# Kernel optimization log

Hardware: AMD Instinct MI355X
Metric: run time of the kernel (lower is better)

## Reference

```python
import jax, jax.numpy as jnp
import numpy as np

N = 100000      # total nodes across the batch of graphs
E = 1600000     # total edges (avg degree 16)
D = 128         # dim_drug (== num_feature here)
L = 3           # layer_drug
G = 2048        # number of graphs in the batch
BN_EPS = 1e-5


def setup_inputs() -> dict:
    key = jax.random.key(0)
    ks = jax.random.split(key, 10)
    x = jax.random.normal(ks[0], (N, D), dtype=jnp.float32)
    edge_index = jax.random.randint(ks[1], (2, E), 0, N, dtype=jnp.int64)
    batch = jnp.sort(jax.random.randint(ks[2], (N,), 0, G, dtype=jnp.int64))
    s = 0.05
    W1 = jax.random.normal(ks[3], (L, D, D), dtype=jnp.float32) * s
    b1 = jax.random.normal(ks[4], (L, D), dtype=jnp.float32) * s
    W2 = jax.random.normal(ks[5], (L, D, D), dtype=jnp.float32) * s
    b2 = jax.random.normal(ks[6], (L, D), dtype=jnp.float32) * s
    gamma = jnp.ones((L, D), dtype=jnp.float32)
    beta = jnp.zeros((L, D), dtype=jnp.float32)
    return {"x": x, "edge_index": edge_index, "batch": batch,
            "W1": W1, "b1": b1, "W2": W2, "b2": b2,
            "gamma": gamma, "beta": beta}


def reference(x, edge_index, batch, W1, b1, W2, b2, gamma, beta):
    src, dst = edge_index[0], edge_index[1]
    h = x
    layer_outs = []
    for i in range(L):
        # GINConv, eps=0: MLP( (1+eps)*h + sum_{j->i} h_j )
        agg = jax.ops.segment_sum(h[src], dst, num_segments=N)  # [N, D]
        m = agg + h
        m = jax.nn.relu(m @ W1[i] + b1[i]) @ W2[i] + b2[i]       # 2-layer MLP
        m = jax.nn.relu(m)                                        # F.relu after conv
        # BatchNorm1d (training mode: batch stats over node dim, biased var)
        mean = jnp.mean(m, axis=0)
        var = jnp.mean((m - mean) ** 2, axis=0)
        h = gamma[i] * (m - mean) * jax.lax.rsqrt(var + BN_EPS) + beta[i]
        layer_outs.append(h)
    node_rep = jnp.concatenate(layer_outs, axis=1)  # JK 'cat' -> [N, L*D]
    return jax.ops.segment_max(node_rep, batch, num_segments=G)  # [G, L*D]
```

## Files before the change

kernel.cpp:

```cpp
#include <hip/hip_runtime.h>
#include <stdint.h>

#define NN 100000
#define NE 1600000
#define DD 128
#define NL 3
#define NG 2048
#define BN_EPS 1e-5f
#define CAP 56
#define GSH 9
#define GSZ 512
#define NGRP 196
#define GBINCAP 9216

typedef short s16x8 __attribute__((ext_vector_type(8)));
typedef float f32x4 __attribute__((ext_vector_type(4)));

__device__ __forceinline__ unsigned short f2bfu(float f) {
    union { float f; unsigned int i; } x; x.f = f;
    unsigned int r = x.i + 0x7fffu + ((x.i >> 16) & 1u);
    return (unsigned short)(r >> 16);
}
__device__ __forceinline__ float bfu2f(unsigned short u) {
    union { unsigned int i; float f; } x; x.i = ((unsigned int)u) << 16; return x.f;
}
__device__ __forceinline__ float uplo(unsigned int u) {
    union { unsigned int i; float f; } x; x.i = u << 16; return x.f;
}
__device__ __forceinline__ float uphi(unsigned int u) {
    union { unsigned int i; float f; } x; x.i = u & 0xffff0000u; return x.f;
}
__device__ __forceinline__ void add8(float* a, uint4 v) {
    a[0] += uplo(v.x); a[1] += uphi(v.x);
    a[2] += uplo(v.y); a[3] += uphi(v.y);
    a[4] += uplo(v.z); a[5] += uphi(v.z);
    a[6] += uplo(v.w); a[7] += uphi(v.w);
}
__device__ __forceinline__ unsigned int pack2(float a, float b) {
    return (unsigned int)f2bfu(a) | ((unsigned int)f2bfu(b) << 16);
}

__global__ __launch_bounds__(256) void k_cvt(
    const float* __restrict__ x, unsigned short* __restrict__ hb)
{
    int i = (blockIdx.x * 256 + threadIdx.x) * 4;
    if (i >= NN * DD) return;
    float4 v = *(const float4*)(x + i);
    ushort4 o;
    o.x = f2bfu(v.x); o.y = f2bfu(v.y); o.z = f2bfu(v.z); o.w = f2bfu(v.w);
    *(ushort4*)(hb + i) = o;
}

__global__ __launch_bounds__(256) void k_wtrans(
    const float* __restrict__ W1, const float* __restrict__ W2,
    unsigned short* __restrict__ Wt)
{
    int idx = blockIdx.x * 256 + threadIdx.x;
    if (idx >= 6 * DD * DD) return;
    int mat = idx >> 14;
    int r = idx & 16383;
    int n = r >> 7, k = r & 127;
    const float* src = (mat < 3) ? (W1 + mat * DD * DD) : (W2 + (mat - 3) * DD * DD);
    Wt[idx] = f2bfu(src[k * DD + n]);
}

__global__ __launch_bounds__(256) void k_bounds(
    const int* __restrict__ batch, int* __restrict__ start)
{
    int n = blockIdx.x * 256 + threadIdx.x;
    if (n >= NN) return;
    int bn = batch[n];
    bn = bn < 0 ? 0 : (bn > NG - 1 ? NG - 1 : bn);
    int bp;
    if (n == 0) bp = -1;
    else {
        bp = batch[n - 1];
        bp = bp < 0 ? 0 : (bp > NG - 1 ? NG - 1 : bp);
    }
    for (int g = bp + 1; g <= bn; ++g) start[g] = n;
    if (n == NN - 1) {
        for (int g = bn + 1; g <= NG; ++g) start[g] = NN;
    }
}

__global__ __launch_bounds__(256) void k_grp(
    const int* __restrict__ ei, int* __restrict__ gcnt,
    unsigned int* __restrict__ bins)
{
    __shared__ int hist[256];
    __shared__ int scn[256];
    __shared__ int exs[256];
    __shared__ int lofs[256];
    __shared__ int gbase[256];
    __shared__ unsigned int stage[4096];
    const int tid = threadIdx.x;
    hist[tid] = 0;
    __syncthreads();

    unsigned int pk[16];
    int gg[16];
    unsigned int vmask = 0;
    #pragma unroll
    for (int q = 0; q < 4; ++q) {
        long long e0 = (long long)blockIdx.x * 4096 + q * 1024 + tid * 4;
        if (e0 < NE) {
            const int* dp = ei + NE + e0;
            const int* sp = ei + e0;
            int dd_[4], ss_[4];
            dd_[0] = __builtin_nontemporal_load(dp + 0);
            dd_[1] = __builtin_nontemporal_load(dp + 1);
            dd_[2] = __builtin_nontemporal_load(dp + 2);
            dd_[3] = __builtin_nontemporal_load(dp + 3);
            ss_[0] = __builtin_nontemporal_load(sp + 0);
            ss_[1] = __builtin_nontemporal_load(sp + 1);
            ss_[2] = __builtin_nontemporal_load(sp + 2);
            ss_[3] = __builtin_nontemporal_load(sp + 3);
            #pragma unroll
            for (int i = 0; i < 4; ++i) {
                int dst = dd_[i], src = ss_[i];
                if ((unsigned)dst < NN && (unsigned)src < NN) {
                    int g = dst >> GSH;
                    int j = q * 4 + i;
                    pk[j] = ((unsigned)(dst & (GSZ - 1)) << 17) | (unsigned)src;
                    gg[j] = g;
                    atomicAdd(&hist[g], 1);
                    vmask |= 1u << j;
                }
            }
        }
    }
    __syncthreads();

    int v = hist[tid];
    scn[tid] = v;
    __syncthreads();
    #pragma unroll
    for (int off = 1; off < 256; off <<= 1) {
        int t = (tid >= off) ? scn[tid - off] : 0;
        __syncthreads();
        scn[tid] += t;
        __syncthreads();
    }
    int ex = scn[tid] - v;
    exs[tid] = ex;
    lofs[tid] = ex;
    if (tid < NGRP) {
        gbase[tid] = hist[tid] ? atomicAdd(&gcnt[tid], hist[tid]) : 0;
    }
    __syncthreads();

    #pragma unroll
    for (int j = 0; j < 16; ++j) {
        if (vmask & (1u << j)) {
            int p = atomicAdd(&lofs[gg[j]], 1);
            stage[p] = pk[j];
        }
    }
    __syncthreads();

    const int wave = tid >> 6, lane = tid & 63;
    for (int g = wave; g < NGRP; g += 4) {
        int len = hist[g];
        if (!len) continue;
        int gb = gbase[g], pb = exs[g];
        for (int k = lane; k < len; k += 64) {
            int o = gb + k;
            if (o < GBINCAP)
                bins[(long long)g * GBINCAP + o] = stage[pb + k];
        }
    }
}

__global__ __launch_bounds__(256, 1) void k_csr(
    const int* __restrict__ gcnt, const unsigned int* __restrict__ bins,
    int* __restrict__ cnt, int* __restrict__ csr)
{
    __shared__ int lcnt[GSZ];
    __shared__ int lcsr[GSZ * CAP];
    const int g = blockIdx.x;
    const int tid = threadIdx.x;
    for (int i = tid; i < GSZ; i += 256) lcnt[i] = 0;
    __syncthreads();

    int count = gcnt[g];
    count = count > GBINCAP ? GBINCAP : count;
    const unsigned int* bp = bins + (long long)g * GBINCAP;
    for (int e = tid * 4; e < count; e += 1024) {
        if (e + 4 <= count) {
            uint4 q4;
            q4.x = __builtin_nontemporal_load(bp + e + 0);
            q4.y = __builtin_nontemporal_load(bp + e + 1);
            q4.z = __builtin_nontemporal_load(bp + e + 2);
            q4.w = __builtin_nontemporal_load(bp + e + 3);
            unsigned int u[4] = {q4.x, q4.y, q4.z, q4.w};
            #pragma unroll
            for (int i = 0; i < 4; ++i) {
                int local = (int)(u[i] >> 17);
                int src = (int)(u[i] & 0x1FFFFu);
                int pos = atomicAdd(&lcnt[local], 1);
                if (pos < CAP) lcsr[local * CAP + pos] = src;
            }
        } else {
            for (int i = e; i < count; ++i) {
                unsigned int u = bp[i];
                int local = (int)(u >> 17);
                int src = (int)(u & 0x1FFFFu);
                int pos = atomicAdd(&lcnt[local], 1);
                if (pos < CAP) lcsr[local * CAP + pos] = src;
            }
        }
    }
    __syncthreads();

    const int nbase = g << GSH;
    int nmax = NN - nbase;
    nmax = nmax > GSZ ? GSZ : nmax;
    for (int i = tid; i < nmax; i += 256) cnt[nbase + i] = lcnt[i];
    const int tot = nmax * CAP;
    int* dstp = csr + (long long)nbase * CAP;
    for (int i = tid * 4; i < tot; i += 1024)
        *(int4*)(dstp + i) = *(const int4*)(&lcsr[i]);
}

__global__ __launch_bounds__(256) void k_agg(
    const unsigned short* __restrict__ hb, const int* __restrict__ cnt,
    const int* __restrict__ csr, unsigned short* __restrict__ aggf)
{
    const int node = blockIdx.x * 16 + (threadIdx.x >> 4);
    const int lane = threadIdx.x & 15;
    if (node >= NN) return;
    int deg = cnt[node];
    deg = deg > CAP ? CAP : deg;
    const int* bkt = csr + node * CAP;
    const unsigned short* base = hb + lane * 8;
    float acc[8];
    {
        uint4 v = *(const uint4*)(base + (long long)node * DD);
        acc[0] = uplo(v.x); acc[1] = uphi(v.x);
        acc[2] = uplo(v.y); acc[3] = uphi(v.y);
        acc[4] = uplo(v.z); acc[5] = uphi(v.z);
        acc[6] = uplo(v.w); acc[7] = uphi(v.w);
    }
    int e = 0;
    for (; e + 8 <= deg; e += 8) {
        int4 i0 = *(const int4*)(bkt + e);
        int4 i1 = *(const int4*)(bkt + e + 4);
        uint4 v0 = *(const uint4*)(base + (long long)i0.x * DD);
        uint4 v1 = *(const uint4*)(base + (long long)i0.y * DD);
        uint4 v2 = *(const uint4*)(base + (long long)i0.z * DD);
        uint4 v3 = *(const uint4*)(base + (long long)i0.w * DD);
        uint4 v4 = *(const uint4*)(base + (long long)i1.x * DD);
        uint4 v5 = *(const uint4*)(base + (long long)i1.y * DD);
        uint4 v6 = *(const uint4*)(base + (long long)i1.z * DD);
        uint4 v7 = *(const uint4*)(base + (long long)i1.w * DD);
        add8(acc, v0); add8(acc, v1); add8(acc, v2); add8(acc, v3);
        add8(acc, v4); add8(acc, v5); add8(acc, v6); add8(acc, v7);
    }
    for (; e + 4 <= deg; e += 4) {
        int4 i0 = *(const int4*)(bkt + e);
        uint4 v0 = *(const uint4*)(base + (long long)i0.x * DD);
        uint4 v1 = *(const uint4*)(base + (long long)i0.y * DD);
        uint4 v2 = *(const uint4*)(base + (long long)i0.z * DD);
        uint4 v3 = *(const uint4*)(base + (long long)i0.w * DD);
        add8(acc, v0); add8(acc, v1); add8(acc, v2); add8(acc, v3);
    }
    for (; e < deg; ++e) {
        uint4 v = *(const uint4*)(base + (long long)bkt[e] * DD);
        add8(acc, v);
    }
    uint4 o;
    o.x = pack2(acc[0], acc[1]);
    o.y = pack2(acc[2], acc[3]);
    o.z = pack2(acc[4], acc[5]);
    o.w = pack2(acc[6], acc[7]);
    *(uint4*)(aggf + (long long)node * DD + lane * 8) = o;
}

__global__ __launch_bounds__(256, 2) void k_mlp(
    const unsigned short* __restrict__ aggf, unsigned short* __restrict__ hb,
    const unsigned short* __restrict__ W1t, const float* __restrict__ b1,
    const unsigned short* __restrict__ W2t, const float* __restrict__ b2,
    float* __restrict__ stats)
{
    __shared__ unsigned short lA[128 * 136];
    __shared__ unsigned short lW[128 * 136];
    __shared__ float sSum[4][128];
    __shared__ float sSq[4][128];
    const int tid = threadIdx.x;
    const int row0 = blockIdx.x * 128;

    #pragma unroll
    for (int it = 0; it < 8; ++it) {
        int eidx = (it * 256 + tid) * 8;
        int r = eidx >> 7, c = eidx & 127;
        *(uint4*)(&lW[r * 136 + c]) = *(const uint4*)(W1t + eidx);
    }
    {
        int col8 = tid & 15, rr = tid >> 4;
        #pragma unroll
        for (int it = 0; it < 8; ++it) {
            int r = rr + it * 16;
            int grow = row0 + r;
            uint4 v;
            if (grow < NN) {
                v = *(const uint4*)(aggf + (long long)grow * DD + col8 * 8);
            } else {
                v.x = v.y = v.z = v.w = 0;
            }
            *(uint4*)(&lA[r * 136 + col8 * 8]) = v;
        }
    }
    __syncthreads();

    const int wave = tid >> 6, lane = tid & 63;
    const int quad = lane >> 4, m16 = lane & 15;

    f32x4 acc[2][8] = {};
    #pragma unroll
    for (int k0 = 0; k0 < 128; k0 += 32) {
        const int kk = k0 + quad * 8;
        s16x8 a0 = *(const s16x8*)(&lA[(wave * 32 + m16) * 136 + kk]);
        s16x8 a1 = *(const s16x8*)(&lA[(wave * 32 + 16 + m16) * 136 + kk]);
        #pragma unroll
        for (int ct = 0; ct < 8; ++ct) {
            s16x8 bf = *(const s16x8*)(&lW[(ct * 16 + m16) * 136 + kk]);
            acc[0][ct] = __builtin_amdgcn_mfma_f32_16x16x32_bf16(a0, bf, acc[0][ct], 0, 0, 0);
            acc[1][ct] = __builtin_amdgcn_mfma_f32_16x16x32_bf16(a1, bf, acc[1][ct], 0, 0, 0);
        }
    }
    __syncthreads();

    #pragma unroll
    for (int rt = 0; rt < 2; ++rt) {
        #pragma unroll
        for (int ct = 0; ct < 8; ++ct) {
            int col = ct * 16 + m16;
            float b = b1[col];
            #pragma unroll
            for (int r = 0; r < 4; ++r) {
                int lrow = wave * 32 + rt * 16 + quad * 4 + r;
                lA[lrow * 136 + col] = f2bfu(fmaxf(acc[rt][ct][r] + b, 0.0f));
            }
        }
    }
    #pragma unroll
    for (int it = 0; it < 8; ++it) {
        int eidx = (it * 256 + tid) * 8;
        int r = eidx >> 7, c = eidx & 127;
        *(uint4*)(&lW[r * 136 + c]) = *(const uint4*)(W2t + eidx);
    }
    __syncthreads();

    #pragma unroll
    for (int rt = 0; rt < 2; ++rt)
        #pragma unroll
        for (int ct = 0; ct < 8; ++ct)
            acc[rt][ct] = f32x4{0.f, 0.f, 0.f, 0.f};
    #pragma unroll
    for (int k0 = 0; k0 < 128; k0 += 32) {
        const int kk = k0 + quad * 8;
        s16x8 a0 = *(const s16x8*)(&lA[(wave * 32 + m16) * 136 + kk]);
        s16x8 a1 = *(const s16x8*)(&lA[(wave * 32 + 16 + m16) * 136 + kk]);
        #pragma unroll
        for (int ct = 0; ct < 8; ++ct) {
            s16x8 bf = *(const s16x8*)(&lW[(ct * 16 + m16) * 136 + kk]);
            acc[0][ct] = __builtin_amdgcn_mfma_f32_16x16x32_bf16(a0, bf, acc[0][ct], 0, 0, 0);
            acc[1][ct] = __builtin_amdgcn_mfma_f32_16x16x32_bf16(a1, bf, acc[1][ct], 0, 0, 0);
        }
    }

    float csum[8] = {}, csq[8] = {};
    #pragma unroll
    for (int rt = 0; rt < 2; ++rt) {
        int rbase = row0 + wave * 32 + rt * 16 + quad * 4;
        #pragma unroll
        for (int ct = 0; ct < 8; ++ct) {
            int col = ct * 16 + m16;
            float b = b2[col];
            #pragma unroll
            for (int r = 0; r < 4; ++r) {
                int row = rbase + r;
                if (row < NN) {
                    float v = fmaxf(acc[rt][ct][r] + b, 0.0f);
                    hb[(long long)row * DD + col] = f2bfu(v);
                    csum[ct] += v;
                    csq[ct] += v * v;
                }
            }
        }
    }
    #pragma unroll
    for (int ct = 0; ct < 8; ++ct) {
        csum[ct] += __shfl_xor(csum[ct], 16);
        csum[ct] += __shfl_xor(csum[ct], 32);
        csq[ct]  += __shfl_xor(csq[ct], 16);
        csq[ct]  += __shfl_xor(csq[ct], 32);
    }
    if (quad == 0) {
        #pragma unroll
        for (int ct = 0; ct < 8; ++ct) {
            int col = ct * 16 + m16;
            sSum[wave][col] = csum[ct];
            sSq[wave][col] = csq[ct];
        }
    }
    __syncthreads();
    if (tid < 128) {
        float s = sSum[0][tid] + sSum[1][tid] + sSum[2][tid] + sSum[3][tid];
        float q = sSq[0][tid] + sSq[1][tid] + sSq[2][tid] + sSq[3][tid];
        atomicAdd(&stats[tid], s);
        atomicAdd(&stats[DD + tid], q);
    }
}

template <bool WR>
__global__ __launch_bounds__(256) void k_norm(
    unsigned short* __restrict__ hb, const float* __restrict__ stats,
    const float* __restrict__ gamma, const float* __restrict__ beta,
    const int* __restrict__ start, float* __restrict__ out, int layer)
{
    __shared__ float sMx[256];
    const int d = threadIdx.x & 127;
    const int half = threadIdx.x >> 7;
    const int g = blockIdx.x;
    const float inv_n = 1.0f / (float)NN;
    float mean = stats[d] * inv_n;
    float var = stats[DD + d] * inv_n - mean * mean;
    float inv = rsqrtf(fmaxf(var, 0.f) + BN_EPS);
    float a = gamma[d] * inv;
    float c = beta[d] - mean * a;
    int n0 = start[g], n1 = start[g + 1];
    n0 = n0 < 0 ? 0 : (n0 > NN ? NN : n0);
    n1 = n1 < 0 ? 0 : (n1 > NN ? NN : n1);
    float mx = -3.0e38f;
    for (int n = n0 + half; n < n1; n += 2) {
        float v = bfu2f(hb[(long long)n * DD + d]);
        float hv = a * v + c;
        if (WR) hb[(long long)n * DD + d] = f2bfu(hv);
        mx = fmaxf(mx, hv);
    }
    sMx[threadIdx.x] = mx;
    __syncthreads();
    if (threadIdx.x < 128) {
        float m = fmaxf(sMx[d], sMx[d + 128]);
        if (n1 <= n0) m = 0.f;
        out[(long long)g * (NL * DD) + layer * DD + d] = m;
    }
}

extern "C" void kernel_launch(void* const* d_in, const int* in_sizes, int n_in,
                              void* d_out, int out_size, void* d_ws, size_t ws_size,
                              hipStream_t stream) {
    const float* x     = (const float*)d_in[0];
    const int*   ei    = (const int*)d_in[1];
    const int*   batch = (const int*)d_in[2];
    const float* W1    = (const float*)d_in[3];
    const float* b1    = (const float*)d_in[4];
    const float* W2    = (const float*)d_in[5];
    const float* b2    = (const float*)d_in[6];
    const float* gamma = (const float*)d_in[7];
    const float* beta  = (const float*)d_in[8];
    float* out = (float*)d_out;
    unsigned short* aggf = (unsigned short*)d_in[0];
    unsigned int*   bins = (unsigned int*)d_in[0];

    char* p = (char*)d_ws;
    float*          stats = (float*)p;
    int*            gcnt  = (int*)(p + 3072);
    int*            cnt   = (int*)(p + 4096);
    int*            start = (int*)(p + 405504);
    unsigned short* Wt    = (unsigned short*)(p + 417792);
    int*            csr   = (int*)(p + 614400);
    unsigned short* hb    = (unsigned short*)(p + 23014400);

    hipMemsetAsync(p, 0, 404096, stream);
    k_cvt<<<(NN * DD / 4 + 255) / 256, 256, 0, stream>>>(x, hb);
    k_wtrans<<<(6 * DD * DD + 255) / 256, 256, 0, stream>>>(W1, W2, Wt);
    k_bounds<<<(NN + 255) / 256, 256, 0, stream>>>(batch, start);
    k_grp<<<(NE + 4095) / 4096, 256, 0, stream>>>(ei, gcnt, bins);
    k_csr<<<NGRP, 256, 0, stream>>>(gcnt, bins, cnt, csr);

    for (int l = 0; l < NL; ++l) {
        float* stats_l = stats + l * 256;
        k_agg<<<(NN + 15) / 16, 256, 0, stream>>>(hb, cnt, csr, aggf);
        k_mlp<<<(NN + 127) / 128, 256, 0, stream>>>(aggf, hb,
                                                    Wt + l * DD * DD, b1 + l * DD,
                                                    Wt + (3 + l) * DD * DD, b2 + l * DD,
                                                    stats_l);
        if (l < NL - 1)
            k_norm<true><<<NG, 256, 0, stream>>>(hb, stats_l, gamma + l * DD,
                                                 beta + l * DD, start, out, l);
        else
            k_norm<false><<<NG, 256, 0, stream>>>(hb, stats_l, gamma + l * DD,
                                                  beta + l * DD, start, out, l);
    }
}
```

Baseline: 501.0 us.

## Fuse aggregation into MLP kernel and fold BatchNorm affine into next layer

Merges the neighbor-sum gather directly into the MLP kernel, writing aggregated rows straight into LDS instead of a global intermediate buffer. The previous layer's BatchNorm is applied algebraically inside the gather (a*sum + c*(deg+1)), so the norm kernel no longer rewrites h and just computes per-graph maxima. Ping-pong buffers replace in-place updates. This removes one global write/read of the aggregate and one h rewrite per layer, but the fused kernel now runs the irregular gather at lower occupancy (launch bounds 256,2 with large LDS), which may limit latency hiding for the gathers.

```diff
diff --git a/kernel.cpp b/kernel.cpp
--- a/kernel.cpp
+++ b/kernel.cpp
@@ -222,92 +222,105 @@
         *(int4*)(dstp + i) = *(const int4*)(&lcsr[i]);
 }
 
-__global__ __launch_bounds__(256) void k_agg(
-    const unsigned short* __restrict__ hb, const int* __restrict__ cnt,
-    const int* __restrict__ csr, unsigned short* __restrict__ aggf)
-{
-    const int node = blockIdx.x * 16 + (threadIdx.x >> 4);
-    const int lane = threadIdx.x & 15;
-    if (node >= NN) return;
-    int deg = cnt[node];
-    deg = deg > CAP ? CAP : deg;
-    const int* bkt = csr + node * CAP;
-    const unsigned short* base = hb + lane * 8;
-    float acc[8];
-    {
-        uint4 v = *(const uint4*)(base + (long long)node * DD);
-        acc[0] = uplo(v.x); acc[1] = uphi(v.x);
-        acc[2] = uplo(v.y); acc[3] = uphi(v.y);
-        acc[4] = uplo(v.z); acc[5] = uphi(v.z);
-        acc[6] = uplo(v.w); acc[7] = uphi(v.w);
-    }
-    int e = 0;
-    for (; e + 8 <= deg; e += 8) {
-        int4 i0 = *(const int4*)(bkt + e);
-        int4 i1 = *(const int4*)(bkt + e + 4);
-        uint4 v0 = *(const uint4*)(base + (long long)i0.x * DD);
-        uint4 v1 = *(const uint4*)(base + (long long)i0.y * DD);
-        uint4 v2 = *(const uint4*)(base + (long long)i0.z * DD);
-        uint4 v3 = *(const uint4*)(base + (long long)i0.w * DD);
-        uint4 v4 = *(const uint4*)(base + (long long)i1.x * DD);
-        uint4 v5 = *(const uint4*)(base + (long long)i1.y * DD);
-        uint4 v6 = *(const uint4*)(base + (long long)i1.z * DD);
-        uint4 v7 = *(const uint4*)(base + (long long)i1.w * DD);
-        add8(acc, v0); add8(acc, v1); add8(acc, v2); add8(acc, v3);
-        add8(acc, v4); add8(acc, v5); add8(acc, v6); add8(acc, v7);
-    }
-    for (; e + 4 <= deg; e += 4) {
-        int4 i0 = *(const int4*)(bkt + e);
-        uint4 v0 = *(const uint4*)(base + (long long)i0.x * DD);
-        uint4 v1 = *(const uint4*)(base + (long long)i0.y * DD);
-        uint4 v2 = *(const uint4*)(base + (long long)i0.z * DD);
-        uint4 v3 = *(const uint4*)(base + (long long)i0.w * DD);
-        add8(acc, v0); add8(acc, v1); add8(acc, v2); add8(acc, v3);
-    }
-    for (; e < deg; ++e) {
-        uint4 v = *(const uint4*)(base + (long long)bkt[e] * DD);
-        add8(acc, v);
-    }
-    uint4 o;
-    o.x = pack2(acc[0], acc[1]);
-    o.y = pack2(acc[2], acc[3]);
-    o.z = pack2(acc[4], acc[5]);
-    o.w = pack2(acc[6], acc[7]);
-    *(uint4*)(aggf + (long long)node * DD + lane * 8) = o;
-}
-
-__global__ __launch_bounds__(256, 2) void k_mlp(
-    const unsigned short* __restrict__ aggf, unsigned short* __restrict__ hb,
+template <bool L0>
+__global__ __launch_bounds__(256, 2) void k_fused(
+    const unsigned short* __restrict__ hin, const int* __restrict__ cnt,
+    const int* __restrict__ csr,
     const unsigned short* __restrict__ W1t, const float* __restrict__ b1,
     const unsigned short* __restrict__ W2t, const float* __restrict__ b2,
-    float* __restrict__ stats)
+    unsigned short* __restrict__ hout, float* __restrict__ stats_out,
+    const float* __restrict__ stats_prev, const float* __restrict__ gamma_prev,
+    const float* __restrict__ beta_prev)
 {
     __shared__ unsigned short lA[128 * 136];
     __shared__ unsigned short lW[128 * 136];
     __shared__ float sSum[4][128];
     __shared__ float sSq[4][128];
+    __shared__ float sAf[128];
+    __shared__ float sCf[128];
     const int tid = threadIdx.x;
     const int row0 = blockIdx.x * 128;
 
+    if (tid < 128) {
+        float a, c;
+        if (L0) { a = 1.0f; c = 0.0f; }
+        else {
+            const float inv_n = 1.0f / (float)NN;
+            float mean = stats_prev[tid] * inv_n;
+            float var = stats_prev[DD + tid] * inv_n - mean * mean;
+            float inv = rsqrtf(fmaxf(var, 0.f) + BN_EPS);
+            a = gamma_prev[tid] * inv;
+            c = beta_prev[tid] - mean * a;
+        }
+        sAf[tid] = a; sCf[tid] = c;
+    }
     #pragma unroll
     for (int it = 0; it < 8; ++it) {
         int eidx = (it * 256 + tid) * 8;
         int r = eidx >> 7, c = eidx & 127;
         *(uint4*)(&lW[r * 136 + c]) = *(const uint4*)(W1t + eidx);
     }
+    __syncthreads();
+
     {
-        int col8 = tid & 15, rr = tid >> 4;
-        #pragma unroll
-        for (int it = 0; it < 8; ++it) {
-            int r = rr + it * 16;
-            int grow = row0 + r;
-            uint4 v;
-            if (grow < NN) {
-                v = *(const uint4*)(aggf + (long long)grow * DD + col8 * 8);
-            } else {
-                v.x = v.y = v.z = v.w = 0;
+        const int grp = tid >> 4, lane = tid & 15;
+        const unsigned short* gbase = hin + lane * 8;
+        float af[8], cf[8];
+        #pragma unroll
+        for (int j = 0; j < 8; ++j) {
+            af[j] = sAf[lane * 8 + j];
+            cf[j] = sCf[lane * 8 + j];
+        }
+        for (int i = 0; i < 8; ++i) {
+            int row = grp * 8 + i;
+            int node = row0 + row;
+            float acc[8] = {};
+            if (node < NN) {
+                int deg = cnt[node];
+                deg = deg > CAP ? CAP : deg;
+                {
+                    uint4 v = *(const uint4*)(gbase + (long long)node * DD);
+                    add8(acc, v);
+                }
+                const int* bkt = csr + node * CAP;
+                int e = 0;
+                for (; e + 8 <= deg; e += 8) {
+                    int4 i0 = *(const int4*)(bkt + e);
+                    int4 i1 = *(const int4*)(bkt + e + 4);
+                    uint4 v0 = *(const uint4*)(gbase + (long long)i0.x * DD);
+                    uint4 v1 = *(const uint4*)(gbase + (long long)i0.y * DD);
+                    uint4 v2 = *(const uint4*)(gbase + (long long)i0.z * DD);
+                    uint4 v3 = *(const uint4*)(gbase + (long long)i0.w * DD);
+                    uint4 v4 = *(const uint4*)(gbase + (long long)i1.x * DD);
+                    uint4 v5 = *(const uint4*)(gbase + (long long)i1.y * DD);
+                    uint4 v6 = *(const uint4*)(gbase + (long long)i1.z * DD);
+                    uint4 v7 = *(const uint4*)(gbase + (long long)i1.w * DD);
+                    add8(acc, v0); add8(acc, v1); add8(acc, v2); add8(acc, v3);
+                    add8(acc, v4); add8(acc, v5); add8(acc, v6); add8(acc, v7);
+                }
+                for (; e + 4 <= deg; e += 4) {
+                    int4 i0 = *(const int4*)(bkt + e);
+                    uint4 v0 = *(const uint4*)(gbase + (long long)i0.x * DD);
+                    uint4 v1 = *(const uint4*)(gbase + (long long)i0.y * DD);
+                    uint4 v2 = *(const uint4*)(gbase + (long long)i0.z * DD);
+                    uint4 v3 = *(const uint4*)(gbase + (long long)i0.w * DD);
+                    add8(acc, v0); add8(acc, v1); add8(acc, v2); add8(acc, v3);
+                }
+                for (; e < deg; ++e) {
+                    uint4 v = *(const uint4*)(gbase + (long long)bkt[e] * DD);
+                    add8(acc, v);
+                }
+                float dp1 = (float)(deg + 1);
+                #pragma unroll
+                for (int j = 0; j < 8; ++j)
+                    acc[j] = af[j] * acc[j] + cf[j] * dp1;
             }
-            *(uint4*)(&lA[r * 136 + col8 * 8]) = v;
+            uint4 o;
+            o.x = pack2(acc[0], acc[1]);
+            o.y = pack2(acc[2], acc[3]);
+            o.z = pack2(acc[4], acc[5]);
+            o.w = pack2(acc[6], acc[7]);
+            *(uint4*)(&lA[row * 136 + lane * 8]) = o;
         }
     }
     __syncthreads();
@@ -382,7 +395,7 @@
                 int row = rbase + r;
                 if (row < NN) {
                     float v = fmaxf(acc[rt][ct][r] + b, 0.0f);
-                    hb[(long long)row * DD + col] = f2bfu(v);
+                    hout[(long long)row * DD + col] = f2bfu(v);
                     csum[ct] += v;
                     csq[ct] += v * v;
                 }
@@ -408,14 +421,13 @@
     if (tid < 128) {
         float s = sSum[0][tid] + sSum[1][tid] + sSum[2][tid] + sSum[3][tid];
         float q = sSq[0][tid] + sSq[1][tid] + sSq[2][tid] + sSq[3][tid];
-        atomicAdd(&stats[tid], s);
-        atomicAdd(&stats[DD + tid], q);
-    }
-}
-
-template <bool WR>
-__global__ __launch_bounds__(256) void k_norm(
-    unsigned short* __restrict__ hb, const float* __restrict__ stats,
+        atomicAdd(&stats_out[tid], s);
+        atomicAdd(&stats_out[DD + tid], q);
+    }
+}
+
+__global__ __launch_bounds__(256) void k_max(
+    const unsigned short* __restrict__ hb, const float* __restrict__ stats,
     const float* __restrict__ gamma, const float* __restrict__ beta,
     const int* __restrict__ start, float* __restrict__ out, int layer)
 {
@@ -435,9 +447,7 @@
     float mx = -3.0e38f;
     for (int n = n0 + half; n < n1; n += 2) {
         float v = bfu2f(hb[(long long)n * DD + d]);
-        float hv = a * v + c;
-        if (WR) hb[(long long)n * DD + d] = f2bfu(hv);
-        mx = fmaxf(mx, hv);
+        mx = fmaxf(mx, a * v + c);
     }
     sMx[threadIdx.x] = mx;
     __syncthreads();
@@ -461,8 +471,8 @@
     const float* gamma = (const float*)d_in[7];
     const float* beta  = (const float*)d_in[8];
     float* out = (float*)d_out;
-    unsigned short* aggf = (unsigned short*)d_in[0];
     unsigned int*   bins = (unsigned int*)d_in[0];
+    unsigned short* hbB  = (unsigned short*)((char*)d_in[0] + 25600000);
 
     char* p = (char*)d_ws;
     float*          stats = (float*)p;
@@ -471,27 +481,35 @@
     int*            start = (int*)(p + 405504);
     unsigned short* Wt    = (unsigned short*)(p + 417792);
     int*            csr   = (int*)(p + 614400);
-    unsigned short* hb    = (unsigned short*)(p + 23014400);
+    unsigned short* hbA   = (unsigned short*)(p + 23014400);
 
     hipMemsetAsync(p, 0, 404096, stream);
-    k_cvt<<<(NN * DD / 4 + 255) / 256, 256, 0, stream>>>(x, hb);
+    k_cvt<<<(NN * DD / 4 + 255) / 256, 256, 0, stream>>>(x, hbA);
     k_wtrans<<<(6 * DD * DD + 255) / 256, 256, 0, stream>>>(W1, W2, Wt);
     k_bounds<<<(NN + 255) / 256, 256, 0, stream>>>(batch, start);
     k_grp<<<(NE + 4095) / 4096, 256, 0, stream>>>(ei, gcnt, bins);
     k_csr<<<NGRP, 256, 0, stream>>>(gcnt, bins, cnt, csr);
 
+    const int nblk = (NN + 127) / 128;
+    unsigned short* hin[NL]  = {hbA, hbB, hbA};
+    unsigned short* hout[NL] = {hbB, hbA, hbB};
     for (int l = 0; l < NL; ++l) {
         float* stats_l = stats + l * 256;
-        k_agg<<<(NN + 15) / 16, 256, 0, stream>>>(hb, cnt, csr, aggf);
-        k_mlp<<<(NN + 127) / 128, 256, 0, stream>>>(aggf, hb,
-                                                    Wt + l * DD * DD, b1 + l * DD,
-                                                    Wt + (3 + l) * DD * DD, b2 + l * DD,
-                                                    stats_l);
-        if (l < NL - 1)
-            k_norm<true><<<NG, 256, 0, stream>>>(hb, stats_l, gamma + l * DD,
-                                                 beta + l * DD, start, out, l);
-        else
-            k_norm<false><<<NG, 256, 0, stream>>>(hb, stats_l, gamma + l * DD,
-                                                  beta + l * DD, start, out, l);
-    }
-}
+        if (l == 0) {
+            k_fused<true><<<nblk, 256, 0, stream>>>(
+                hin[l], cnt, csr,
+                Wt + l * DD * DD, b1 + l * DD,
+                Wt + (3 + l) * DD * DD, b2 + l * DD,
+                hout[l], stats_l, nullptr, nullptr, nullptr);
+        } else {
+            k_fused<false><<<nblk, 256, 0, stream>>>(
+                hin[l], cnt, csr,
+                Wt + l * DD * DD, b1 + l * DD,
+                Wt + (3 + l) * DD * DD, b2 + l * DD,
+                hout[l], stats_l,
+                stats + (l - 1) * 256, gamma + (l - 1) * DD, beta + (l - 1) * DD);
+        }
+        k_max<<<NG, 256, 0, stream>>>(hout[l], stats_l, gamma + l * DD,
+                                      beta + l * DD, start, out, l);
+    }
+}
```

New measurement: 518.2 us. +3.4%, slower.

## Fold BatchNorm into next-layer aggregation and fuse segment max/min into MLP

Applied to the files above, without the earlier changes.

Removes the per-layer normalization kernel. The affine BN transform is applied algebraically inside the next layer's aggregation (a*sum + c*(deg+1)). Per-graph max and min of the pre-norm activations are gathered in the MLP epilogue through LDS and global atomics, and a final small kernel picks max or min according to the sign of the BN scale. This saves one full read/write pass over the activations per layer, at the cost of atomic traffic, extra memsets, and some bf16 rounding differences from applying the affine after the sum.

```diff
diff --git a/kernel.cpp b/kernel.cpp
--- a/kernel.cpp
+++ b/kernel.cpp
@@ -12,6 +12,7 @@
 #define GSZ 512
 #define NGRP 196
 #define GBINCAP 9216
+#define MAXSEG 16
 
 typedef short s16x8 __attribute__((ext_vector_type(8)));
 typedef float f32x4 __attribute__((ext_vector_type(4)));
@@ -222,13 +223,32 @@
         *(int4*)(dstp + i) = *(const int4*)(&lcsr[i]);
 }
 
+template <bool L0>
 __global__ __launch_bounds__(256) void k_agg(
     const unsigned short* __restrict__ hb, const int* __restrict__ cnt,
-    const int* __restrict__ csr, unsigned short* __restrict__ aggf)
+    const int* __restrict__ csr, unsigned short* __restrict__ aggf,
+    const float* __restrict__ stats_prev, const float* __restrict__ gamma_prev,
+    const float* __restrict__ beta_prev)
 {
     const int node = blockIdx.x * 16 + (threadIdx.x >> 4);
     const int lane = threadIdx.x & 15;
     if (node >= NN) return;
+    float af[8], cf[8];
+    if (L0) {
+        #pragma unroll
+        for (int j = 0; j < 8; ++j) { af[j] = 1.0f; cf[j] = 0.0f; }
+    } else {
+        const float inv_n = 1.0f / (float)NN;
+        #pragma unroll
+        for (int j = 0; j < 8; ++j) {
+            int d = lane * 8 + j;
+            float mean = stats_prev[d] * inv_n;
+            float var = stats_prev[DD + d] * inv_n - mean * mean;
+            float inv = rsqrtf(fmaxf(var, 0.f) + BN_EPS);
+            af[j] = gamma_prev[d] * inv;
+            cf[j] = beta_prev[d] - mean * af[j];
+        }
+    }
     int deg = cnt[node];
     deg = deg > CAP ? CAP : deg;
     const int* bkt = csr + node * CAP;
@@ -268,6 +288,12 @@
         uint4 v = *(const uint4*)(base + (long long)bkt[e] * DD);
         add8(acc, v);
     }
+    if (!L0) {
+        float dp1 = (float)(deg + 1);
+        #pragma unroll
+        for (int j = 0; j < 8; ++j)
+            acc[j] = af[j] * acc[j] + cf[j] * dp1;
+    }
     uint4 o;
     o.x = pack2(acc[0], acc[1]);
     o.y = pack2(acc[2], acc[3]);
@@ -276,19 +302,28 @@
     *(uint4*)(aggf + (long long)node * DD + lane * 8) = o;
 }
 
+template <bool WRH>
 __global__ __launch_bounds__(256, 2) void k_mlp(
-    const unsigned short* __restrict__ aggf, unsigned short* __restrict__ hb,
+    const unsigned short* __restrict__ aggf, unsigned short* __restrict__ hout,
     const unsigned short* __restrict__ W1t, const float* __restrict__ b1,
     const unsigned short* __restrict__ W2t, const float* __restrict__ b2,
-    float* __restrict__ stats)
+    float* __restrict__ stats, const int* __restrict__ batch,
+    unsigned int* __restrict__ gmxl, unsigned int* __restrict__ gmnl)
 {
     __shared__ unsigned short lA[128 * 136];
     __shared__ unsigned short lW[128 * 136];
     __shared__ float sSum[4][128];
     __shared__ float sSq[4][128];
+    __shared__ int sB[128];
     const int tid = threadIdx.x;
     const int row0 = blockIdx.x * 128;
 
+    if (tid < 128) {
+        int row = row0 + tid;
+        int b = batch[row < NN ? row : NN - 1];
+        b = b < 0 ? 0 : (b > NG - 1 ? NG - 1 : b);
+        sB[tid] = b;
+    }
     #pragma unroll
     for (int it = 0; it < 8; ++it) {
         int eidx = (it * 256 + tid) * 8;
@@ -368,23 +403,63 @@
             acc[1][ct] = __builtin_amdgcn_mfma_f32_16x16x32_bf16(a1, bf, acc[1][ct], 0, 0, 0);
         }
     }
+    __syncthreads();
+
+    unsigned int* lseg = (unsigned int*)lA;
+    for (int i = tid; i < 2048; i += 256) {
+        lseg[i] = 0u;
+        lseg[i + 2048] = 0x7f7f7f7fu;
+    }
+    __syncthreads();
+
+    const int g_first = sB[0];
+    int nvalid = NN - row0; nvalid = nvalid > 128 ? 128 : nvalid;
+    const int nseg = sB[nvalid - 1] - g_first + 1;
+    const bool ldsok = (nseg <= MAXSEG);
 
     float csum[8] = {}, csq[8] = {};
     #pragma unroll
     for (int rt = 0; rt < 2; ++rt) {
-        int rbase = row0 + wave * 32 + rt * 16 + quad * 4;
+        int lbase = wave * 32 + rt * 16 + quad * 4;
+        int rbase = row0 + lbase;
         #pragma unroll
         for (int ct = 0; ct < 8; ++ct) {
             int col = ct * 16 + m16;
             float b = b2[col];
+            int sprev = -1;
+            float rmx = 0.f, rmn = 0.f;
             #pragma unroll
             for (int r = 0; r < 4; ++r) {
                 int row = rbase + r;
                 if (row < NN) {
                     float v = fmaxf(acc[rt][ct][r] + b, 0.0f);
-                    hb[(long long)row * DD + col] = f2bfu(v);
+                    if (WRH) hout[(long long)row * DD + col] = f2bfu(v);
                     csum[ct] += v;
                     csq[ct] += v * v;
+                    int s = sB[lbase + r] - g_first;
+                    if (s == sprev) {
+                        rmx = fmaxf(rmx, v); rmn = fminf(rmn, v);
+                    } else {
+                        if (sprev >= 0) {
+                            if (ldsok) {
+                                atomicMax(&lseg[sprev * 128 + col], __float_as_uint(rmx));
+                                atomicMin(&lseg[2048 + sprev * 128 + col], __float_as_uint(rmn));
+                            } else {
+                                atomicMax(&gmxl[(g_first + sprev) * DD + col], __float_as_uint(rmx));
+                                atomicMin(&gmnl[(g_first + sprev) * DD + col], __float_as_uint(rmn));
+                            }
+                        }
+                        sprev = s; rmx = v; rmn = v;
+                    }
+                }
+            }
+            if (sprev >= 0) {
+                if (ldsok) {
+                    atomicMax(&lseg[sprev * 128 + col], __float_as_uint(rmx));
+                    atomicMin(&lseg[2048 + sprev * 128 + col], __float_as_uint(rmn));
+                } else {
+                    atomicMax(&gmxl[(g_first + sprev) * DD + col], __float_as_uint(rmx));
+                    atomicMin(&gmnl[(g_first + sprev) * DD + col], __float_as_uint(rmn));
                 }
             }
         }
@@ -405,6 +480,14 @@
         }
     }
     __syncthreads();
+    if (ldsok) {
+        for (int i = tid; i < nseg * 128; i += 256) {
+            int g = g_first + (i >> 7), col = i & 127;
+            unsigned int um = lseg[i], un = lseg[2048 + i];
+            if (um) atomicMax(&gmxl[g * DD + col], um);
+            if (un != 0x7f7f7f7fu) atomicMin(&gmnl[g * DD + col], un);
+        }
+    }
     if (tid < 128) {
         float s = sSum[0][tid] + sSum[1][tid] + sSum[2][tid] + sSum[3][tid];
         float q = sSq[0][tid] + sSq[1][tid] + sSq[2][tid] + sSq[3][tid];
@@ -413,39 +496,32 @@
     }
 }
 
-template <bool WR>
-__global__ __launch_bounds__(256) void k_norm(
-    unsigned short* __restrict__ hb, const float* __restrict__ stats,
-    const float* __restrict__ gamma, const float* __restrict__ beta,
-    const int* __restrict__ start, float* __restrict__ out, int layer)
-{
-    __shared__ float sMx[256];
-    const int d = threadIdx.x & 127;
-    const int half = threadIdx.x >> 7;
-    const int g = blockIdx.x;
+__global__ __launch_bounds__(256) void k_out(
+    const float* __restrict__ stats, const float* __restrict__ gamma,
+    const float* __restrict__ beta, const int* __restrict__ start,
+    const unsigned int* __restrict__ gmx, const unsigned int* __restrict__ gmn,
+    float* __restrict__ out)
+{
+    int idx = blockIdx.x * 256 + threadIdx.x;
+    if (idx >= NL * NG * DD) return;
+    int l = idx / (NG * DD);
+    int rem = idx - l * NG * DD;
+    int g = rem >> 7;
+    int d = rem & 127;
     const float inv_n = 1.0f / (float)NN;
-    float mean = stats[d] * inv_n;
-    float var = stats[DD + d] * inv_n - mean * mean;
+    float mean = stats[l * 256 + d] * inv_n;
+    float var = stats[l * 256 + DD + d] * inv_n - mean * mean;
     float inv = rsqrtf(fmaxf(var, 0.f) + BN_EPS);
-    float a = gamma[d] * inv;
-    float c = beta[d] - mean * a;
+    float a = gamma[l * DD + d] * inv;
+    float c = beta[l * DD + d] - mean * a;
     int n0 = start[g], n1 = start[g + 1];
-    n0 = n0 < 0 ? 0 : (n0 > NN ? NN : n0);
-    n1 = n1 < 0 ? 0 : (n1 > NN ? NN : n1);
-    float mx = -3.0e38f;
-    for (int n = n0 + half; n < n1; n += 2) {
-        float v = bfu2f(hb[(long long)n * DD + d]);
-        float hv = a * v + c;
-        if (WR) hb[(long long)n * DD + d] = f2bfu(hv);
-        mx = fmaxf(mx, hv);
-    }
-    sMx[threadIdx.x] = mx;
-    __syncthreads();
-    if (threadIdx.x < 128) {
-        float m = fmaxf(sMx[d], sMx[d + 128]);
-        if (n1 <= n0) m = 0.f;
-        out[(long long)g * (NL * DD) + layer * DD + d] = m;
-    }
+    float res = 0.f;
+    if (n1 > n0) {
+        float mx = __uint_as_float(gmx[(l * NG + g) * DD + d]);
+        float mn = __uint_as_float(gmn[(l * NG + g) * DD + d]);
+        res = (a >= 0.f) ? fmaf(a, mx, c) : fmaf(a, mn, c);
+    }
+    out[(long long)g * (NL * DD) + l * DD + d] = res;
 }
 
 extern "C" void kernel_launch(void* const* d_in, const int* in_sizes, int n_in,
@@ -462,7 +538,9 @@
     const float* beta  = (const float*)d_in[8];
     float* out = (float*)d_out;
     unsigned short* aggf = (unsigned short*)d_in[0];
-    unsigned int*   bins = (unsigned int*)d_in[0];
+    unsigned int*   bins = (unsigned int*)((char*)d_in[0] + 25600000);
+    unsigned int*   gmx  = (unsigned int*)((char*)d_in[0] + 32825344);
+    unsigned int*   gmn  = (unsigned int*)((char*)d_in[0] + 35971072);
 
     char* p = (char*)d_ws;
     float*          stats = (float*)p;
@@ -475,23 +553,36 @@
 
     hipMemsetAsync(p, 0, 404096, stream);
     k_cvt<<<(NN * DD / 4 + 255) / 256, 256, 0, stream>>>(x, hb);
+    hipMemsetAsync(gmx, 0x00, NL * NG * DD * 4, stream);
+    hipMemsetAsync(gmn, 0x7f, NL * NG * DD * 4, stream);
     k_wtrans<<<(6 * DD * DD + 255) / 256, 256, 0, stream>>>(W1, W2, Wt);
     k_bounds<<<(NN + 255) / 256, 256, 0, stream>>>(batch, start);
     k_grp<<<(NE + 4095) / 4096, 256, 0, stream>>>(ei, gcnt, bins);
     k_csr<<<NGRP, 256, 0, stream>>>(gcnt, bins, cnt, csr);
 
+    const int nblk = (NN + 127) / 128;
     for (int l = 0; l < NL; ++l) {
         float* stats_l = stats + l * 256;
-        k_agg<<<(NN + 15) / 16, 256, 0, stream>>>(hb, cnt, csr, aggf);
-        k_mlp<<<(NN + 127) / 128, 256, 0, stream>>>(aggf, hb,
-                                                    Wt + l * DD * DD, b1 + l * DD,
-                                                    Wt + (3 + l) * DD * DD, b2 + l * DD,
-                                                    stats_l);
+        unsigned int* gmxl = gmx + l * NG * DD;
+        unsigned int* gmnl = gmn + l * NG * DD;
+        if (l == 0)
+            k_agg<true><<<(NN + 15) / 16, 256, 0, stream>>>(
+                hb, cnt, csr, aggf, nullptr, nullptr, nullptr);
+        else
+            k_agg<false><<<(NN + 15) / 16, 256, 0, stream>>>(
+                hb, cnt, csr, aggf,
+                stats + (l - 1) * 256, gamma + (l - 1) * DD, beta + (l - 1) * DD);
         if (l < NL - 1)
-            k_norm<true><<<NG, 256, 0, stream>>>(hb, stats_l, gamma + l * DD,
-                                                 beta + l * DD, start, out, l);
+            k_mlp<true><<<nblk, 256, 0, stream>>>(
+                aggf, hb, Wt + l * DD * DD, b1 + l * DD,
+                Wt + (3 + l) * DD * DD, b2 + l * DD,
+                stats_l, batch, gmxl, gmnl);
         else
-            k_norm<false><<<NG, 256, 0, stream>>>(hb, stats_l, gamma + l * DD,
-                                                  beta + l * DD, start, out, l);
-    }
-}
+            k_mlp<false><<<nblk, 256, 0, stream>>>(
+                aggf, hb, Wt + l * DD * DD, b1 + l * DD,
+                Wt + (3 + l) * DD * DD, b2 + l * DD,
+                stats_l, batch, gmxl, gmnl);
+    }
+    k_out<<<(NL * NG * DD + 255) / 256, 256, 0, stream>>>(
+        stats, gamma, beta, start, gmx, gmn, out);
+}
```

Result: no change. 502.2 us (+0.2%).
